# Kernel tuning notes

Measured on AMD Instinct MI355X. Metric: run time of the kernel, lower is better.

Reference implementation:

```python
import jax, jax.numpy as jnp
import numpy as np

B, T, S, O = 8, 60, 36, 1
H, E, PE = 4, 16, 16
AD, TA, OUT, L = 12, 10, 64, 2
PRUNE_KEEP_FROM = int(np.floor(S * S * 0.5))  # floor(S^2 * (1 - prune_rate))
EPS = 1e-5


def lrelu(v):
    return jax.nn.leaky_relu(v, 0.01)


def pos_encode(times):
    # standard sinusoidal PE on raw timestamps -> (B, T, PE)
    half = PE // 2
    div = jnp.exp(jnp.arange(half, dtype=jnp.float32) * (-jnp.log(10000.0) / half))
    ang = times[..., None] * div
    return jnp.stack([jnp.sin(ang), jnp.cos(ang)], axis=-1).reshape(times.shape + (PE,))


def pair_sim(adj):
    # sum_{i<j} ||a_i - a_j||^2 = B*sum_i||a_i||^2 - ||sum_i a_i||^2
    b = adj.shape[0]
    sq = jnp.sum(adj * adj)
    tot = jnp.sum(adj, axis=0)
    return (b * sq - jnp.sum(tot * tot)) / ((b - 1) ** 2) / (S * S)


def _forward(x, times, mask, bn_g, bn_b, obs_emb_w, attn_w, bidir_w, proj_W, proj_b,
             Wq, bq, Wk, bk, Ws, bs, lnt_g, lnt_b, Wse, bse, lns_g, lns_b):
    b = x.shape[0]
    # BatchNorm2d over timestep channels (training-mode batch stats)
    mu = x.mean(axis=(0, 2, 3), keepdims=True)
    var = x.var(axis=(0, 2, 3), keepdims=True)
    x = (x - mu) / jnp.sqrt(var + EPS) * bn_g[None, :, None, None] + bn_b[None, :, None, None]
    # per-sensor observation embedding: (B,T,S,O) x (S,O,E*H) -> (B,H,T,S,E)
    h = lrelu(jnp.einsum('btso,som->btsm', x, obs_emb_w))
    h = h.reshape(b, T, S, H, E).transpose(0, 3, 1, 2, 4)
    h = h * mask[:, None, :, :, None]
    pe = pos_encode(times)  # (B,T,PE)
    adj = jnp.ones((b, H, S, S), x.dtype)
    sim = pair_sim(adj)  # 0 for all-ones init, kept for faithfulness
    prune_msk = None
    for lay in range(L):
        hp = h @ proj_W.T + proj_b  # (B,H,T,S,AD+PE)
        cat = jnp.concatenate([
            jnp.broadcast_to(attn_w[lay][None, :, None], (b, H, T, S, AD)),
            jnp.broadcast_to(pe[:, None, :, None], (b, H, T, S, PE))], axis=-1)
        alpha = lrelu(jnp.einsum('bhtsd,bhtjd->bhtsj', hp, cat))  # (B,H,T,S,S)
        if lay:
            cnt = mask.sum(axis=1)[:, None, :, None]  # (B,1,S,1)
            adj = lrelu(adj * (alpha.sum(axis=2) / cnt))
            if prune_msk is None:
                flat = adj.reshape(b, H, S * S)
                ranks = jnp.argsort(jnp.argsort(flat, axis=-1), axis=-1)
                prune_msk = (ranks >= PRUNE_KEEP_FROM).astype(adj.dtype).reshape(b, H, S, S)
            adj = adj * prune_msk
            sim = sim + pair_sim(adj)
        bidir = lrelu(jnp.einsum('hsd,hjd->hsj', bidir_w[lay], bidir_w[lay]))  # (H,S,S)
        w = lrelu(bidir[None, :, None] * alpha * adj[:, :, None])  # (B,H,T,S,S)
        # broadcast message passing: (B,H,T,1,S,E) * (B,H,T,S,S,1) -> sum over source sensor
        h = lrelu(jnp.sum(lrelu(h[:, :, :, None, :, :] * w[..., None]), axis=4))
    pe_e = jnp.broadcast_to(pe[:, None, :, None], (b, H, T, S, PE))
    Hc = jnp.concatenate([h, pe_e], axis=-1).transpose(0, 1, 3, 2, 4)  # (B,H,S,T,E+PE)
    Q = Hc @ Wq.T + bq
    K = Hc @ Wk.T + bk
    beta = jnp.einsum('bhstd,bhsud->bhstu', Q, K)  # (B,H,S,T,T)
    beta = (beta @ Ws.T + bs)[..., 0]  # (B,H,S,T)
    m = beta.mean(axis=(-2, -1), keepdims=True)
    v = beta.var(axis=(-2, -1), keepdims=True)
    beta = (beta - m) / jnp.sqrt(v + EPS) * lnt_g + lnt_b
    out = lrelu(jnp.einsum('bhst,bhstd->bhsd', beta, Hc))
    out = lrelu(out @ Wse.T + bse)
    m2 = out.mean(axis=(-2, -1), keepdims=True)
    v2 = out.var(axis=(-2, -1), keepdims=True)
    out = (out - m2) / jnp.sqrt(v2 + EPS) * lns_g + lns_b
    out = out.transpose(0, 2, 1, 3).reshape(b, S, OUT)
    return out, sim


def setup_inputs():
    key = jax.random.key(0)
    ks = jax.random.split(key, 12)
    def rn(k, shape, scale=0.1):
        return jax.random.normal(k, shape, jnp.float32) * scale
    return {
        'x': jax.random.normal(ks[0], (B, T, S, O), jnp.float32),
        'times': jnp.tile(jnp.arange(T, dtype=jnp.float32), (B, 1)),
        'mask': jnp.ones((B, T, S), jnp.float32),
        'bn_g': jnp.ones((T,), jnp.float32),
        'bn_b': jnp.zeros((T,), jnp.float32),
        'obs_emb_w': rn(ks[1], (S, O, E * H)),
        'attn_w': rn(ks[2], (L, H, S, AD)),
        'bidir_w': rn(ks[3], (L, H, S, AD)),
        'proj_W': rn(ks[4], (AD + PE, E)),
        'proj_b': jnp.zeros((AD + PE,), jnp.float32),
        'Wq': rn(ks[5], (TA, E + PE)),
        'bq': jnp.zeros((TA,), jnp.float32),
        'Wk': rn(ks[6], (TA, E + PE)),
        'bk': jnp.zeros((TA,), jnp.float32),
        'Ws': rn(ks[7], (1, T)),
        'bs': jnp.zeros((1,), jnp.float32),
        'lnt_g': jnp.ones((S, T), jnp.float32),
        'lnt_b': jnp.zeros((S, T), jnp.float32),
        'Wse': rn(ks[8], (OUT // H, E + PE)),
        'bse': jnp.zeros((OUT // H,), jnp.float32),
        'lns_g': jnp.ones((S, OUT // H), jnp.float32),
        'lns_b': jnp.zeros((S, OUT // H), jnp.float32),
    }


def reference(x, times, mask, bn_g, bn_b, obs_emb_w, attn_w, bidir_w, proj_W, proj_b,
              Wq, bq, Wk, bk, Ws, bs, lnt_g, lnt_b, Wse, bse, lns_g, lns_b):
    return _forward(x, times, mask, bn_g, bn_b, obs_emb_w, attn_w, bidir_w, proj_W, proj_b,
                    Wq, bq, Wk, bk, Ws, bs, lnt_g, lnt_b, Wse, bse, lns_g, lns_b)
```

## Files before the change

### kernel.cpp

```cpp
#include <hip/hip_runtime.h>
#include <math.h>

#define Bc 8
#define Tc 60
#define Sc 36
#define Hc_ 4
#define Ec 16
#define PEc 16
#define ADc 12
#define TAc 10
#define OUTc 64
#define KEEP 648
#define EPSc 1e-5f
#define LOG1E4_8 1.15129254649702284f

#define WS_H2     18176
#define WS_H1     1124096
#define WS_ALPHA  2230016
#define WS_ADJ    4759808
#define WS_ADJP   4801280
#define WS_CNT    5050112
#define WS_BETA   WS_ALPHA
#define WS_PART   (WS_ALPHA + 69120)
#define WS_OUT2   (WS_ALPHA + 71424)
#define WS_PART2  (WS_ALPHA + 89856)

__device__ __forceinline__ float lrelu(float v){ return v >= 0.f ? v : 0.01f*v; }

__global__ __launch_bounds__(256) void k_layer01(const float* __restrict__ x,
                          const float* __restrict__ times,
                          const float* __restrict__ mask,
                          const float* __restrict__ bn_g,
                          const float* __restrict__ bn_b,
                          const float* __restrict__ obs_w,
                          const float* __restrict__ attn,
                          const float* __restrict__ bidw,
                          const float* __restrict__ projW,
                          const float* __restrict__ projb,
                          float* __restrict__ ws){
    int idx = blockIdx.x;
    int t = idx % Tc; int bh = idx / Tc; int h = bh % Hc_; int b = bh / Hc_;
    int tid = threadIdx.x;
    __shared__ float sh_h[Sc*Ec];
    __shared__ float sh_h1[Sc*Ec];
    __shared__ float sh_pe[PEc];
    __shared__ float sh_at0T[ADc*Sc];
    __shared__ float sh_at1T[ADc*Sc];
    __shared__ float sh_bwT[ADc*Sc];
    __shared__ float sh_hp[Sc*28];
    __shared__ float sh_P[Sc];
    __shared__ float sh_w[Sc*Sc];
    __shared__ float sh_xn[Sc];
    __shared__ float sh_m[Sc];
    __shared__ float sred[8];
    float s0 = 0.f, s1 = 0.f;
    for (int i = tid; i < Bc*Sc; i += 256){
        float v = x[((i/Sc)*Tc + t)*Sc + (i%Sc)];
        s0 += v; s1 += v*v;
    }
    #pragma unroll
    for (int off = 32; off; off >>= 1){
        s0 += __shfl_down(s0, off, 64);
        s1 += __shfl_down(s1, off, 64);
    }
    if ((tid & 63) == 0){ sred[(tid>>6)*2] = s0; sred[(tid>>6)*2 + 1] = s1; }
    if (tid >= 64 && tid < 80){
        int q = tid - 64; int j = q >> 1;
        float ang = times[b*Tc + t] * expf(-(float)j * LOG1E4_8);
        sh_pe[q] = (q & 1) ? cosf(ang) : sinf(ang);
    }
    for (int i = tid; i < ADc*Sc; i += 256){
        int d = i / Sc, j = i % Sc;
        sh_at0T[i] = attn[h*Sc*ADc + j*ADc + d];
        sh_at1T[i] = attn[(Hc_ + h)*Sc*ADc + j*ADc + d];
        sh_bwT[i]  = bidw[h*Sc*ADc + j*ADc + d];
    }
    __syncthreads();
    float mu  = (sred[0]+sred[2]+sred[4]+sred[6]) / (float)(Bc*Sc);
    float var = (sred[1]+sred[3]+sred[5]+sred[7]) / (float)(Bc*Sc) - mu*mu;
    if (tid < Sc){
        float xv = x[(b*Tc + t)*Sc + tid];
        sh_xn[tid] = (xv - mu) * rsqrtf(var + EPSc) * bn_g[t] + bn_b[t];
        sh_m[tid]  = mask[(b*Tc + t)*Sc + tid];
    }
    __syncthreads();
    for (int i = tid; i < Sc*Ec; i += 256){
        int s = i / Ec, e = i % Ec;
        sh_h[i] = lrelu(sh_xn[s]*obs_w[s*64 + h*Ec + e]) * sh_m[s];
    }
    __syncthreads();
    for (int i = tid; i < Sc*28; i += 256){
        int s = i / 28, d = i % 28;
        float acc = projb[d];
        const float* w = projW + d*Ec;
        const float* hh = sh_h + s*Ec;
        #pragma unroll
        for (int e = 0; e < Ec; e++) acc += hh[e]*w[e];
        sh_hp[i] = acc;
    }
    __syncthreads();
    if (tid < Sc){
        const float* hp = sh_hp + tid*28 + ADc;
        float p = 0.f;
        #pragma unroll
        for (int d = 0; d < PEc; d++) p += hp[d]*sh_pe[d];
        sh_P[tid] = p;
    }
    __syncthreads();
    for (int i = tid; i < Sc*Sc; i += 256){
        int s = i / Sc, j = i % Sc;
        const float* hp = sh_hp + s*28;
        float acc = sh_P[s];
        float bd = 0.f;
        #pragma unroll
        for (int d = 0; d < ADc; d++){
            acc += hp[d]*sh_at0T[d*Sc + j];
            bd  += sh_bwT[d*Sc + s]*sh_bwT[d*Sc + j];
        }
        sh_w[i] = lrelu(lrelu(bd)*lrelu(acc));
    }
    __syncthreads();
    float* h1g = ws + WS_H1 + (size_t)idx*Sc*Ec;
    for (int i = tid; i < Sc*Ec; i += 256){
        int s = i / Ec, e = i % Ec;
        float acc = 0.f;
        #pragma unroll 6
        for (int j = 0; j < Sc; j++) acc += lrelu(sh_h[j*Ec + e]*sh_w[s*Sc + j]);
        float v = lrelu(acc);
        sh_h1[i] = v;
        h1g[i] = v;
    }
    __syncthreads();
    for (int i = tid; i < Sc*28; i += 256){
        int s = i / 28, d = i % 28;
        float acc = projb[d];
        const float* w = projW + d*Ec;
        const float* hh = sh_h1 + s*Ec;
        #pragma unroll
        for (int e = 0; e < Ec; e++) acc += hh[e]*w[e];
        sh_hp[i] = acc;
    }
    __syncthreads();
    if (tid < Sc){
        const float* hp = sh_hp + tid*28 + ADc;
        float p = 0.f;
        #pragma unroll
        for (int d = 0; d < PEc; d++) p += hp[d]*sh_pe[d];
        sh_P[tid] = p;
    }
    __syncthreads();
    float* adst = ws + WS_ALPHA + (size_t)idx*Sc*Sc;
    for (int i = tid; i < Sc*Sc; i += 256){
        int s = i / Sc, j = i % Sc;
        const float* hp = sh_hp + s*28;
        float acc = sh_P[s];
        #pragma unroll
        for (int d = 0; d < ADc; d++) acc += hp[d]*sh_at1T[d*Sc + j];
        adst[i] = lrelu(acc);
    }
}

__global__ __launch_bounds__(256) void k_adjpart(const float* __restrict__ mask, float* __restrict__ ws){
    int bh = blockIdx.x / 6; int chunk = blockIdx.x % 6;
    int tid = threadIdx.x;
    const float4* a = (const float4*)(ws + WS_ALPHA + (size_t)bh*Tc*Sc*Sc) + (size_t)chunk*10*324;
    float4* p = (float4*)(ws + WS_ADJP + (size_t)blockIdx.x*Sc*Sc);
    for (int c = tid; c < 324; c += 256){
        float4 acc = make_float4(0.f, 0.f, 0.f, 0.f);
        #pragma unroll
        for (int tt = 0; tt < 10; tt++){
            float4 u = a[(size_t)tt*324 + c];
            acc.x += u.x; acc.y += u.y; acc.z += u.z; acc.w += u.w;
        }
        p[c] = acc;
    }
    if (chunk == 0 && (bh & 3) == 0 && tid < Sc){
        int b = bh >> 2;
        float c = 0.f;
        #pragma unroll 4
        for (int t = 0; t < Tc; t++) c += mask[(b*Tc + t)*Sc + tid];
        ws[WS_CNT + b*Sc + tid] = c;
    }
}

__global__ __launch_bounds__(256) void k_prune(float* __restrict__ ws){
    int bh = blockIdx.x / 24; int chunk = blockIdx.x % 24;
    int b = bh >> 2;
    int tid = threadIdx.x;
    __shared__ __align__(16) float sh_v[Sc*Sc];
    __shared__ float sh_cnt[Sc];
    const float4* p = (const float4*)(ws + WS_ADJP + (size_t)bh*6*Sc*Sc);
    for (int c = tid; c < 324; c += 256){
        float4 acc = make_float4(0.f, 0.f, 0.f, 0.f);
        #pragma unroll
        for (int q = 0; q < 6; q++){
            float4 u = p[(size_t)q*324 + c];
            acc.x += u.x; acc.y += u.y; acc.z += u.z; acc.w += u.w;
        }
        ((float4*)sh_v)[c] = acc;
    }
    if (tid < Sc) sh_cnt[tid] = ws[WS_CNT + b*Sc + tid];
    __syncthreads();
    for (int i = tid; i < Sc*Sc; i += 256){
        int s = i / Sc;
        sh_v[i] = lrelu(sh_v[i] / sh_cnt[s]);
    }
    __syncthreads();
    int r = tid >> 2; if (r > 53) r = 53;
    int part = tid & 3;
    int i = chunk*54 + r;
    float v = sh_v[i];
    const float4* v4 = (const float4*)sh_v + part*81;
    int a0 = part*324;
    int cnt = 0;
    #pragma unroll 9
    for (int j = 0; j < 81; j++){
        float4 u = v4[j];
        int k = a0 + j*4;
        cnt += (int)(u.x < v) + ((int)(u.x == v) & (int)(k   < i));
        cnt += (int)(u.y < v) + ((int)(u.y == v) & (int)(k+1 < i));
        cnt += (int)(u.z < v) + ((int)(u.z == v) & (int)(k+2 < i));
        cnt += (int)(u.w < v) + ((int)(u.w == v) & (int)(k+3 < i));
    }
    cnt += __shfl_down(cnt, 2, 4);
    cnt += __shfl_down(cnt, 1, 4);
    if (part == 0 && tid < 216)
        ws[WS_ADJ + bh*Sc*Sc + i] = (cnt >= KEEP) ? v : 0.f;
}

__global__ __launch_bounds__(256) void k_layer1mp(const float* __restrict__ bidw,
                                                  float* __restrict__ ws){
    int idx = blockIdx.x;
    int bh = idx / Tc; int h = bh % Hc_;
    int tid = threadIdx.x;
    __shared__ float sh_h[Sc*Ec];
    __shared__ float sh_w[Sc*Sc];
    __shared__ float sh_bwT[ADc*Sc];
    const float* hsrc = ws + WS_H1 + (size_t)idx*Sc*Ec;
    float*       hdst = ws + WS_H2 + (size_t)idx*Sc*Ec;
    const float* al  = ws + WS_ALPHA + (size_t)idx*Sc*Sc;
    const float* adj = ws + WS_ADJ + bh*Sc*Sc;
    for (int i = tid; i < Sc*Ec; i += 256) sh_h[i] = hsrc[i];
    for (int i = tid; i < ADc*Sc; i += 256){
        int d = i / Sc, j = i % Sc;
        sh_bwT[i] = bidw[(Hc_ + h)*Sc*ADc + j*ADc + d];
    }
    __syncthreads();
    for (int i = tid; i < Sc*Sc; i += 256){
        int s = i / Sc, j = i % Sc;
        float bd = 0.f;
        #pragma unroll
        for (int d = 0; d < ADc; d++) bd += sh_bwT[d*Sc + s]*sh_bwT[d*Sc + j];
        sh_w[i] = lrelu(lrelu(bd)*al[i]*adj[i]);
    }
    __syncthreads();
    for (int i = tid; i < Sc*Ec; i += 256){
        int s = i / Ec, e = i % Ec;
        float acc = 0.f;
        #pragma unroll 6
        for (int j = 0; j < Sc; j++) acc += lrelu(sh_h[j*Ec + e]*sh_w[s*Sc + j]);
        hdst[i] = lrelu(acc);
    }
}

__global__ __launch_bounds__(64) void kF1(const float* __restrict__ Wq, const float* __restrict__ bq,
                   const float* __restrict__ Wk, const float* __restrict__ bk,
                   const float* __restrict__ Ws_, const float* __restrict__ bs_,
                   const float* __restrict__ times, float* __restrict__ ws){
    int idx = blockIdx.x;
    int s = idx % Sc; int bh = idx / Sc; int b = bh / Hc_;
    int tid = threadIdx.x;
    __shared__ float sh_Hc[Tc*33];
    __shared__ float sh_K[Tc*11];
    __shared__ float sh_Wq[TAc*32];
    __shared__ float sh_WkT[32*TAc];
    __shared__ float sh_bq[TAc], sh_bk[TAc];
    __shared__ float sh_ws[Tc];
    __shared__ float sh_Kw[TAc];
    const float* h2 = ws + WS_H2 + (size_t)bh*Tc*Sc*Ec + s*Ec;
    for (int i4 = tid; i4 < Tc*4; i4 += 64){
        int t = i4 >> 2, c4 = i4 & 3;
        float4 u = *(const float4*)(h2 + t*Sc*Ec + c4*4);
        float* d = sh_Hc + t*33 + c4*4;
        d[0] = u.x; d[1] = u.y; d[2] = u.z; d[3] = u.w;
    }
    for (int i = tid; i < Tc*PEc; i += 64){
        int t = i / PEc, q = i % PEc; int j = q >> 1;
        float ang = times[b*Tc + t] * expf(-(float)j * LOG1E4_8);
        sh_Hc[t*33 + Ec + q] = (q & 1) ? cosf(ang) : sinf(ang);
    }
    for (int i = tid; i < TAc*32; i += 64){
        sh_Wq[i] = Wq[i];
        int d = i / 32, q = i % 32;
        sh_WkT[q*TAc + d] = Wk[i];
    }
    if (tid < TAc){ sh_bq[tid] = bq[tid]; sh_bk[tid] = bk[tid]; }
    if (tid < Tc) sh_ws[tid] = Ws_[tid];
    __syncthreads();
    for (int i = tid; i < Tc*TAc; i += 64){
        int t = i / TAc, d = i % TAc;
        const float* hc = sh_Hc + t*33;
        float acc = sh_bk[d];
        #pragma unroll
        for (int q = 0; q < 32; q++) acc += hc[q]*sh_WkT[q*TAc + d];
        sh_K[t*11 + d] = acc;
    }
    __syncthreads();
    if (tid < TAc){
        float acc = 0.f;
        #pragma unroll 4
        for (int t = 0; t < Tc; t++) acc += sh_K[t*11 + tid]*sh_ws[t];
        sh_Kw[tid] = acc;
    }
    __syncthreads();
    float bv = 0.f;
    float bsv = bs_[0];
    if (tid < Tc){
        const float* hc = sh_Hc + tid*33;
        float acc = bsv;
        #pragma unroll
        for (int d = 0; d < TAc; d++){
            const float* wq = sh_Wq + d*32;
            float qv = sh_bq[d];
            #pragma unroll
            for (int q = 0; q < 32; q++) qv += hc[q]*wq[q];
            acc += qv*sh_Kw[d];
        }
        bv = acc;
        ws[WS_BETA + idx*Tc + tid] = acc;
    }
    float p0 = (tid < Tc) ? bv : 0.f;
    float p1 = p0*bv;
    #pragma unroll
    for (int off = 32; off; off >>= 1){
        p0 += __shfl_down(p0, off, 64);
        p1 += __shfl_down(p1, off, 64);
    }
    if (tid == 0){
        ws[WS_PART + idx*2]     = p0;
        ws[WS_PART + idx*2 + 1] = p1;
    }
}

__global__ __launch_bounds__(64) void kF2(const float* __restrict__ lnt_g, const float* __restrict__ lnt_b,
                   const float* __restrict__ Wse, const float* __restrict__ bse,
                   const float* __restrict__ times, float* __restrict__ ws){
    int idx = blockIdx.x;
    int s = idx % Sc; int bh = idx / Sc; int b = bh / Hc_;
    int tid = threadIdx.x;
    __shared__ float sh_Hc[Tc*33];
    __shared__ float sh_beta[Tc];
    __shared__ float sh_o1[32];
    __shared__ float sh_mi[2];
    float p0 = 0.f, p1 = 0.f;
    if (tid < Sc){
        p0 = ws[WS_PART + (bh*Sc + tid)*2];
        p1 = ws[WS_PART + (bh*Sc + tid)*2 + 1];
    }
    #pragma unroll
    for (int off = 32; off; off >>= 1){
        p0 += __shfl_down(p0, off, 64);
        p1 += __shfl_down(p1, off, 64);
    }
    if (tid == 0){
        float m = p0 / (float)(Sc*Tc);
        sh_mi[0] = m;
        sh_mi[1] = rsqrtf(p1 / (float)(Sc*Tc) - m*m + EPSc);
    }
    const float* h2 = ws + WS_H2 + (size_t)bh*Tc*Sc*Ec + s*Ec;
    for (int i4 = tid; i4 < Tc*4; i4 += 64){
        int t = i4 >> 2, c4 = i4 & 3;
        float4 u = *(const float4*)(h2 + t*Sc*Ec + c4*4);
        float* d = sh_Hc + t*33 + c4*4;
        d[0] = u.x; d[1] = u.y; d[2] = u.z; d[3] = u.w;
    }
    for (int i = tid; i < Tc*PEc; i += 64){
        int t = i / PEc, q = i % PEc; int j = q >> 1;
        float ang = times[b*Tc + t] * expf(-(float)j * LOG1E4_8);
        sh_Hc[t*33 + Ec + q] = (q & 1) ? cosf(ang) : sinf(ang);
    }
    __syncthreads();
    float m = sh_mi[0], inv = sh_mi[1];
    if (tid < Tc){
        float bvv = ws[WS_BETA + idx*Tc + tid];
        sh_beta[tid] = (bvv - m)*inv*lnt_g[s*Tc + tid] + lnt_b[s*Tc + tid];
    }
    __syncthreads();
    if (tid < 32){
        float acc = 0.f;
        #pragma unroll 4
        for (int t = 0; t < Tc; t++) acc += sh_beta[t]*sh_Hc[t*33 + tid];
        sh_o1[tid] = lrelu(acc);
    }
    __syncthreads();
    float v = 0.f;
    if (tid < 16){
        float acc = bse[tid];
        const float* w = Wse + tid*32;
        #pragma unroll
        for (int d = 0; d < 32; d++) acc += sh_o1[d]*w[d];
        v = lrelu(acc);
        ws[WS_OUT2 + idx*16 + tid] = v;
    }
    float q0 = v, q1 = v*v;
    #pragma unroll
    for (int off = 32; off; off >>= 1){
        q0 += __shfl_down(q0, off, 64);
        q1 += __shfl_down(q1, off, 64);
    }
    if (tid == 0){
        ws[WS_PART2 + idx*2]     = q0;
        ws[WS_PART2 + idx*2 + 1] = q1;
    }
}

__global__ __launch_bounds__(256) void kF3s(const float* __restrict__ lns_g, const float* __restrict__ lns_b,
                    const float* __restrict__ ws, float* __restrict__ out){
    int tid = threadIdx.x;
    if (blockIdx.x == 32){
        float sq = 0.f, t2 = 0.f;
        for (int i = tid; i < Hc_*Sc*Sc; i += 256){
            float tot = 0.f;
            #pragma unroll
            for (int b = 0; b < Bc; b++){
                float v = ws[WS_ADJ + b*Hc_*Sc*Sc + i];
                sq += v*v; tot += v;
            }
            t2 += tot*tot;
        }
        __shared__ float r0[256], r1[256];
        r0[tid] = sq; r1[tid] = t2; __syncthreads();
        for (int off = 128; off; off >>= 1){
            if (tid < off){ r0[tid] += r0[tid+off]; r1[tid] += r1[tid+off]; }
            __syncthreads();
        }
        if (tid == 0)
            out[Bc*Sc*OUTc] = ((float)Bc*r0[0] - r1[0]) / 49.f / 1296.f;
        return;
    }
    int bh = blockIdx.x; int h = bh % Hc_; int b = bh / Hc_;
    __shared__ float sh_mi[2];
    if (tid < 64){
        float p0 = 0.f, p1 = 0.f;
        if (tid < Sc){
            p0 = ws[WS_PART2 + (bh*Sc + tid)*2];
            p1 = ws[WS_PART2 + (bh*Sc + tid)*2 + 1];
        }
        #pragma unroll
        for (int off = 32; off; off >>= 1){
            p0 += __shfl_down(p0, off, 64);
            p1 += __shfl_down(p1, off, 64);
        }
        if (tid == 0){
            float m = p0 / (float)(Sc*16);
            sh_mi[0] = m;
            sh_mi[1] = rsqrtf(p1 / (float)(Sc*16) - m*m + EPSc);
        }
    }
    __syncthreads();
    float m2 = sh_mi[0], inv2 = sh_mi[1];
    for (int i = tid; i < Sc*16; i += 256){
        int s = i / 16, k = i % 16;
        float v = ws[WS_OUT2 + bh*Sc*16 + i];
        out[(b*Sc + s)*OUTc + h*16 + k] = (v - m2)*inv2*lns_g[i] + lns_b[i];
    }
}

extern "C" void kernel_launch(void* const* d_in, const int* in_sizes, int n_in,
                              void* d_out, int out_size, void* d_ws, size_t ws_size,
                              hipStream_t stream){
    const float* x     = (const float*)d_in[0];
    const float* times = (const float*)d_in[1];
    const float* mask  = (const float*)d_in[2];
    const float* bn_g  = (const float*)d_in[3];
    const float* bn_b  = (const float*)d_in[4];
    const float* obs   = (const float*)d_in[5];
    const float* attn  = (const float*)d_in[6];
    const float* bidw  = (const float*)d_in[7];
    const float* projW = (const float*)d_in[8];
    const float* projb = (const float*)d_in[9];
    const float* Wq    = (const float*)d_in[10];
    const float* bq    = (const float*)d_in[11];
    const float* Wk    = (const float*)d_in[12];
    const float* bk    = (const float*)d_in[13];
    const float* Ws_   = (const float*)d_in[14];
    const float* bs_   = (const float*)d_in[15];
    const float* lnt_g = (const float*)d_in[16];
    const float* lnt_b = (const float*)d_in[17];
    const float* Wse   = (const float*)d_in[18];
    const float* bse   = (const float*)d_in[19];
    const float* lns_g = (const float*)d_in[20];
    const float* lns_b = (const float*)d_in[21];
    float* ws  = (float*)d_ws;
    float* out = (float*)d_out;

    k_layer01<<<Bc*Hc_*Tc, 256, 0, stream>>>(x, times, mask, bn_g, bn_b, obs, attn, bidw, projW, projb, ws);
    k_adjpart<<<Bc*Hc_*6, 256, 0, stream>>>(mask, ws);
    k_prune<<<Bc*Hc_*24, 256, 0, stream>>>(ws);
    k_layer1mp<<<Bc*Hc_*Tc, 256, 0, stream>>>(bidw, ws);
    kF1<<<Bc*Hc_*Sc, 64, 0, stream>>>(Wq, bq, Wk, bk, Ws_, bs_, times, ws);
    kF2<<<Bc*Hc_*Sc, 64, 0, stream>>>(lnt_g, lnt_b, Wse, bse, times, ws);
    kF3s<<<Bc*Hc_ + 1, 256, 0, stream>>>(lns_g, lns_b, ws, out);
}
```

Measured before the change: 207.3 us.

## Fuse seven stage kernels into one persistent cooperative kernel with grid syncs

Replaces the chain of seven kernel launches with a single cooperative kernel of 512 persistent blocks that loops over each stage's work items and separates stages with grid-wide syncs. The goal is to remove per-launch overhead and inter-kernel gaps, which matter because each stage is small. In exchange, each stage runs on a fixed 512-block grid with a grid barrier between stages, and occupancy is capped by launch bounds and a large static shared-memory buffer. If the cooperative launch fails, it falls back to the original multi-kernel path.

```diff
diff --git a/kernel.cpp b/kernel.cpp
--- a/kernel.cpp
+++ b/kernel.cpp
@@ -1,5 +1,8 @@
 #include <hip/hip_runtime.h>
+#include <hip/hip_cooperative_groups.h>
 #include <math.h>
+
+namespace cg = cooperative_groups;
 
 #define Bc 8
 #define Tc 60
@@ -25,7 +28,456 @@
 #define WS_OUT2   (WS_ALPHA + 71424)
 #define WS_PART2  (WS_ALPHA + 89856)
 
+#define GRIDN 512
+
+#define P5_WQ   0
+#define P5_WKT  320
+#define P5_BQ   640
+#define P5_BK   650
+#define P5_WS   660
+#define P5_WAVE 720
+#define SMEM_FLOATS 11392
+
 __device__ __forceinline__ float lrelu(float v){ return v >= 0.f ? v : 0.01f*v; }
+
+__global__ __launch_bounds__(256, 2) void k_fused(
+    const float* __restrict__ x, const float* __restrict__ times,
+    const float* __restrict__ mask, const float* __restrict__ bn_g,
+    const float* __restrict__ bn_b, const float* __restrict__ obs_w,
+    const float* __restrict__ attn, const float* __restrict__ bidw,
+    const float* __restrict__ projW, const float* __restrict__ projb,
+    const float* __restrict__ Wq, const float* __restrict__ bq,
+    const float* __restrict__ Wk, const float* __restrict__ bk,
+    const float* __restrict__ Ws_, const float* __restrict__ bs_,
+    const float* __restrict__ lnt_g, const float* __restrict__ lnt_b,
+    const float* __restrict__ Wse, const float* __restrict__ bse,
+    const float* __restrict__ lns_g, const float* __restrict__ lns_b,
+    float* __restrict__ ws, float* __restrict__ out)
+{
+    cg::grid_group gridg = cg::this_grid();
+    int tid = threadIdx.x;
+    int wid = tid >> 6, lane = tid & 63;
+    __shared__ __align__(16) float smem[SMEM_FLOATS];
+
+    {
+        float* sh_h    = smem;
+        float* sh_h1   = smem + 576;
+        float* sh_pe   = smem + 1152;
+        float* sh_at0T = smem + 1168;
+        float* sh_at1T = smem + 1600;
+        float* sh_bwT  = smem + 2032;
+        float* sh_hp   = smem + 2464;
+        float* sh_P    = smem + 3472;
+        float* sh_w    = smem + 3508;
+        float* sh_xn   = smem + 4804;
+        float* sh_m    = smem + 4840;
+        float* sred    = smem + 4876;
+        for (int u = blockIdx.x; u < Bc*Hc_*Tc; u += GRIDN){
+            __syncthreads();
+            int t = u % Tc; int bh0 = u / Tc; int h = bh0 % Hc_; int b = bh0 / Hc_;
+            float s0 = 0.f, s1 = 0.f;
+            for (int i = tid; i < Bc*Sc; i += 256){
+                float v = x[((i/Sc)*Tc + t)*Sc + (i%Sc)];
+                s0 += v; s1 += v*v;
+            }
+            #pragma unroll
+            for (int off = 32; off; off >>= 1){
+                s0 += __shfl_down(s0, off, 64);
+                s1 += __shfl_down(s1, off, 64);
+            }
+            if ((tid & 63) == 0){ sred[(tid>>6)*2] = s0; sred[(tid>>6)*2 + 1] = s1; }
+            if (tid >= 64 && tid < 80){
+                int q = tid - 64; int j = q >> 1;
+                float ang = times[b*Tc + t] * expf(-(float)j * LOG1E4_8);
+                sh_pe[q] = (q & 1) ? cosf(ang) : sinf(ang);
+            }
+            for (int i = tid; i < ADc*Sc; i += 256){
+                int d = i / Sc, j = i % Sc;
+                sh_at0T[i] = attn[h*Sc*ADc + j*ADc + d];
+                sh_at1T[i] = attn[(Hc_ + h)*Sc*ADc + j*ADc + d];
+                sh_bwT[i]  = bidw[h*Sc*ADc + j*ADc + d];
+            }
+            __syncthreads();
+            float mu  = (sred[0]+sred[2]+sred[4]+sred[6]) / (float)(Bc*Sc);
+            float var = (sred[1]+sred[3]+sred[5]+sred[7]) / (float)(Bc*Sc) - mu*mu;
+            if (tid < Sc){
+                float xv = x[(b*Tc + t)*Sc + tid];
+                sh_xn[tid] = (xv - mu) * rsqrtf(var + EPSc) * bn_g[t] + bn_b[t];
+                sh_m[tid]  = mask[(b*Tc + t)*Sc + tid];
+            }
+            __syncthreads();
+            for (int i = tid; i < Sc*Ec; i += 256){
+                int s = i / Ec, e = i % Ec;
+                sh_h[i] = lrelu(sh_xn[s]*obs_w[s*64 + h*Ec + e]) * sh_m[s];
+            }
+            __syncthreads();
+            for (int i = tid; i < Sc*28; i += 256){
+                int s = i / 28, d = i % 28;
+                float acc = projb[d];
+                const float* w = projW + d*Ec;
+                const float* hh = sh_h + s*Ec;
+                #pragma unroll
+                for (int e = 0; e < Ec; e++) acc += hh[e]*w[e];
+                sh_hp[i] = acc;
+            }
+            __syncthreads();
+            if (tid < Sc){
+                const float* hp = sh_hp + tid*28 + ADc;
+                float p = 0.f;
+                #pragma unroll
+                for (int d = 0; d < PEc; d++) p += hp[d]*sh_pe[d];
+                sh_P[tid] = p;
+            }
+            __syncthreads();
+            for (int i = tid; i < Sc*Sc; i += 256){
+                int s = i / Sc, j = i % Sc;
+                const float* hp = sh_hp + s*28;
+                float acc = sh_P[s];
+                float bd = 0.f;
+                #pragma unroll
+                for (int d = 0; d < ADc; d++){
+                    acc += hp[d]*sh_at0T[d*Sc + j];
+                    bd  += sh_bwT[d*Sc + s]*sh_bwT[d*Sc + j];
+                }
+                sh_w[i] = lrelu(lrelu(bd)*lrelu(acc));
+            }
+            __syncthreads();
+            float* h1g = ws + WS_H1 + (size_t)u*Sc*Ec;
+            for (int i = tid; i < Sc*Ec; i += 256){
+                int s = i / Ec, e = i % Ec;
+                float acc = 0.f;
+                #pragma unroll 6
+                for (int j = 0; j < Sc; j++) acc += lrelu(sh_h[j*Ec + e]*sh_w[s*Sc + j]);
+                float v = lrelu(acc);
+                sh_h1[i] = v;
+                h1g[i] = v;
+            }
+            __syncthreads();
+            for (int i = tid; i < Sc*28; i += 256){
+                int s = i / 28, d = i % 28;
+                float acc = projb[d];
+                const float* w = projW + d*Ec;
+                const float* hh = sh_h1 + s*Ec;
+                #pragma unroll
+                for (int e = 0; e < Ec; e++) acc += hh[e]*w[e];
+                sh_hp[i] = acc;
+            }
+            __syncthreads();
+            if (tid < Sc){
+                const float* hp = sh_hp + tid*28 + ADc;
+                float p = 0.f;
+                #pragma unroll
+                for (int d = 0; d < PEc; d++) p += hp[d]*sh_pe[d];
+                sh_P[tid] = p;
+            }
+            __syncthreads();
+            float* adst = ws + WS_ALPHA + (size_t)u*Sc*Sc;
+            for (int i = tid; i < Sc*Sc; i += 256){
+                int s = i / Sc, j = i % Sc;
+                const float* hp = sh_hp + s*28;
+                float acc = sh_P[s];
+                #pragma unroll
+                for (int d = 0; d < ADc; d++) acc += hp[d]*sh_at1T[d*Sc + j];
+                adst[i] = lrelu(acc);
+            }
+        }
+    }
+    gridg.sync();
+
+    for (int u = blockIdx.x; u < Bc*Hc_*6; u += GRIDN){
+        int bh0 = u / 6; int chunk = u % 6;
+        const float4* a = (const float4*)(ws + WS_ALPHA + (size_t)bh0*Tc*Sc*Sc) + (size_t)chunk*10*324;
+        float4* p = (float4*)(ws + WS_ADJP + (size_t)u*Sc*Sc);
+        for (int c = tid; c < 324; c += 256){
+            float4 acc = make_float4(0.f, 0.f, 0.f, 0.f);
+            #pragma unroll
+            for (int tt = 0; tt < 10; tt++){
+                float4 uu = a[(size_t)tt*324 + c];
+                acc.x += uu.x; acc.y += uu.y; acc.z += uu.z; acc.w += uu.w;
+            }
+            p[c] = acc;
+        }
+        if (chunk == 0 && (bh0 & 3) == 0 && tid < Sc){
+            int b = bh0 >> 2;
+            float c = 0.f;
+            #pragma unroll 4
+            for (int t = 0; t < Tc; t++) c += mask[(b*Tc + t)*Sc + tid];
+            ws[WS_CNT + b*Sc + tid] = c;
+        }
+    }
+    gridg.sync();
+
+    {
+        float* sh_v   = smem;
+        float* sh_cnt = smem + 1296;
+        for (int u = blockIdx.x; u < Bc*Hc_*24; u += GRIDN){
+            __syncthreads();
+            int bh0 = u / 24; int chunk = u % 24;
+            int b = bh0 >> 2;
+            const float4* p = (const float4*)(ws + WS_ADJP + (size_t)bh0*6*Sc*Sc);
+            for (int c = tid; c < 324; c += 256){
+                float4 acc = make_float4(0.f, 0.f, 0.f, 0.f);
+                #pragma unroll
+                for (int q = 0; q < 6; q++){
+                    float4 uu = p[(size_t)q*324 + c];
+                    acc.x += uu.x; acc.y += uu.y; acc.z += uu.z; acc.w += uu.w;
+                }
+                ((float4*)sh_v)[c] = acc;
+            }
+            if (tid < Sc) sh_cnt[tid] = ws[WS_CNT + b*Sc + tid];
+            __syncthreads();
+            for (int i = tid; i < Sc*Sc; i += 256){
+                int s = i / Sc;
+                sh_v[i] = lrelu(sh_v[i] / sh_cnt[s]);
+            }
+            __syncthreads();
+            int r = tid >> 2; if (r > 53) r = 53;
+            int part = tid & 3;
+            int i = chunk*54 + r;
+            float v = sh_v[i];
+            const float4* v4 = (const float4*)sh_v + part*81;
+            int a0 = part*324;
+            int cnt = 0;
+            #pragma unroll 9
+            for (int j = 0; j < 81; j++){
+                float4 uu = v4[j];
+                int k = a0 + j*4;
+                cnt += (int)(uu.x < v) + ((int)(uu.x == v) & (int)(k   < i));
+                cnt += (int)(uu.y < v) + ((int)(uu.y == v) & (int)(k+1 < i));
+                cnt += (int)(uu.z < v) + ((int)(uu.z == v) & (int)(k+2 < i));
+                cnt += (int)(uu.w < v) + ((int)(uu.w == v) & (int)(k+3 < i));
+            }
+            cnt += __shfl_down(cnt, 2, 4);
+            cnt += __shfl_down(cnt, 1, 4);
+            if (part == 0 && tid < 216)
+                ws[WS_ADJ + bh0*Sc*Sc + i] = (cnt >= KEEP) ? v : 0.f;
+        }
+    }
+    gridg.sync();
+
+    {
+        float* sh_h   = smem;
+        float* sh_w   = smem + 576;
+        float* sh_bwT = smem + 1872;
+        for (int u = blockIdx.x; u < Bc*Hc_*Tc; u += GRIDN){
+            __syncthreads();
+            int bh0 = u / Tc; int h = bh0 % Hc_;
+            const float* hsrc = ws + WS_H1 + (size_t)u*Sc*Ec;
+            float*       hdst = ws + WS_H2 + (size_t)u*Sc*Ec;
+            const float* al   = ws + WS_ALPHA + (size_t)u*Sc*Sc;
+            const float* adj  = ws + WS_ADJ + bh0*Sc*Sc;
+            for (int i = tid; i < Sc*Ec; i += 256) sh_h[i] = hsrc[i];
+            for (int i = tid; i < ADc*Sc; i += 256){
+                int d = i / Sc, j = i % Sc;
+                sh_bwT[i] = bidw[(Hc_ + h)*Sc*ADc + j*ADc + d];
+            }
+            __syncthreads();
+            for (int i = tid; i < Sc*Sc; i += 256){
+                int s = i / Sc, j = i % Sc;
+                float bd = 0.f;
+                #pragma unroll
+                for (int d = 0; d < ADc; d++) bd += sh_bwT[d*Sc + s]*sh_bwT[d*Sc + j];
+                sh_w[i] = lrelu(lrelu(bd)*al[i]*adj[i]);
+            }
+            __syncthreads();
+            for (int i = tid; i < Sc*Ec; i += 256){
+                int s = i / Ec, e = i % Ec;
+                float acc = 0.f;
+                #pragma unroll 6
+                for (int j = 0; j < Sc; j++) acc += lrelu(sh_h[j*Ec + e]*sh_w[s*Sc + j]);
+                hdst[i] = lrelu(acc);
+            }
+        }
+    }
+    gridg.sync();
+
+    {
+        __syncthreads();
+        for (int i = tid; i < TAc*32; i += 256){
+            smem[P5_WQ + i] = Wq[i];
+            int d = i / 32, q = i % 32;
+            smem[P5_WKT + q*TAc + d] = Wk[i];
+        }
+        if (tid < TAc){ smem[P5_BQ + tid] = bq[tid]; smem[P5_BK + tid] = bk[tid]; }
+        for (int i = tid; i < Tc; i += 256) smem[P5_WS + i] = Ws_[i];
+        __syncthreads();
+        float* W_Hc = smem + P5_WAVE + wid*2656;
+        float* W_K  = W_Hc + 1980;
+        float* W_Kw = W_Hc + 2640;
+        for (int u = blockIdx.x; u < 288; u += GRIDN){
+            int idx = u*4 + wid;
+            int s = idx % Sc; int bh0 = idx / Sc; int b = bh0 / Hc_;
+            const float* h2 = ws + WS_H2 + (size_t)bh0*Tc*Sc*Ec + s*Ec;
+            for (int i4 = lane; i4 < Tc*4; i4 += 64){
+                int t = i4 >> 2, c4 = i4 & 3;
+                float4 uu = *(const float4*)(h2 + t*Sc*Ec + c4*4);
+                float* d = W_Hc + t*33 + c4*4;
+                d[0] = uu.x; d[1] = uu.y; d[2] = uu.z; d[3] = uu.w;
+            }
+            for (int i = lane; i < Tc*PEc; i += 64){
+                int t = i / PEc, q = i % PEc; int j = q >> 1;
+                float ang = times[b*Tc + t] * expf(-(float)j * LOG1E4_8);
+                W_Hc[t*33 + Ec + q] = (q & 1) ? cosf(ang) : sinf(ang);
+            }
+            __syncthreads();
+            for (int i = lane; i < Tc*TAc; i += 64){
+                int t = i / TAc, d = i % TAc;
+                const float* hc = W_Hc + t*33;
+                float acc = smem[P5_BK + d];
+                #pragma unroll
+                for (int q = 0; q < 32; q++) acc += hc[q]*smem[P5_WKT + q*TAc + d];
+                W_K[t*11 + d] = acc;
+            }
+            __syncthreads();
+            if (lane < TAc){
+                float acc = 0.f;
+                #pragma unroll 4
+                for (int t = 0; t < Tc; t++) acc += W_K[t*11 + lane]*smem[P5_WS + t];
+                W_Kw[lane] = acc;
+            }
+            __syncthreads();
+            float bv = 0.f;
+            float bsv = bs_[0];
+            if (lane < Tc){
+                const float* hc = W_Hc + lane*33;
+                float acc = bsv;
+                #pragma unroll
+                for (int d = 0; d < TAc; d++){
+                    const float* wq = smem + P5_WQ + d*32;
+                    float qv = smem[P5_BQ + d];
+                    #pragma unroll
+                    for (int q = 0; q < 32; q++) qv += hc[q]*wq[q];
+                    acc += qv*W_Kw[d];
+                }
+                bv = acc;
+                ws[WS_BETA + idx*Tc + lane] = acc;
+            }
+            float p0 = (lane < Tc) ? bv : 0.f;
+            float p1 = p0*bv;
+            #pragma unroll
+            for (int off = 32; off; off >>= 1){
+                p0 += __shfl_down(p0, off, 64);
+                p1 += __shfl_down(p1, off, 64);
+            }
+            if (lane == 0){
+                ws[WS_PART + idx*2]     = p0;
+                ws[WS_PART + idx*2 + 1] = p1;
+            }
+        }
+    }
+    gridg.sync();
+
+    {
+        float* W_Hc   = smem + P5_WAVE + wid*2656;
+        float* W_beta = W_Hc + 1980;
+        float* W_o1   = W_Hc + 2040;
+        float* W_mi   = W_Hc + 2072;
+        for (int u = blockIdx.x; u < 288; u += GRIDN){
+            int idx = u*4 + wid;
+            int s = idx % Sc; int bh0 = idx / Sc;
+            float p0 = 0.f, p1 = 0.f;
+            if (lane < Sc){
+                p0 = ws[WS_PART + (bh0*Sc + lane)*2];
+                p1 = ws[WS_PART + (bh0*Sc + lane)*2 + 1];
+            }
+            #pragma unroll
+            for (int off = 32; off; off >>= 1){
+                p0 += __shfl_down(p0, off, 64);
+                p1 += __shfl_down(p1, off, 64);
+            }
+            if (lane == 0){
+                float m = p0 / (float)(Sc*Tc);
+                W_mi[0] = m;
+                W_mi[1] = rsqrtf(p1 / (float)(Sc*Tc) - m*m + EPSc);
+            }
+            __syncthreads();
+            float m = W_mi[0], inv = W_mi[1];
+            if (lane < Tc){
+                float bvv = ws[WS_BETA + idx*Tc + lane];
+                W_beta[lane] = (bvv - m)*inv*lnt_g[s*Tc + lane] + lnt_b[s*Tc + lane];
+            }
+            __syncthreads();
+            if (lane < 32){
+                float acc = 0.f;
+                #pragma unroll 4
+                for (int t = 0; t < Tc; t++) acc += W_beta[t]*W_Hc[t*33 + lane];
+                W_o1[lane] = lrelu(acc);
+            }
+            __syncthreads();
+            float v = 0.f;
+            if (lane < 16){
+                float acc = bse[lane];
+                const float* w = Wse + lane*32;
+                #pragma unroll
+                for (int d = 0; d < 32; d++) acc += W_o1[d]*w[d];
+                v = lrelu(acc);
+                ws[WS_OUT2 + idx*16 + lane] = v;
+            }
+            float q0 = v, q1 = v*v;
+            #pragma unroll
+            for (int off = 32; off; off >>= 1){
+                q0 += __shfl_down(q0, off, 64);
+                q1 += __shfl_down(q1, off, 64);
+            }
+            if (lane == 0){
+                ws[WS_PART2 + idx*2]     = q0;
+                ws[WS_PART2 + idx*2 + 1] = q1;
+            }
+        }
+    }
+    gridg.sync();
+
+    for (int u = blockIdx.x; u < Bc*Hc_ + 1; u += GRIDN){
+        __syncthreads();
+        if (u == 32){
+            float sq = 0.f, t2 = 0.f;
+            for (int i = tid; i < Hc_*Sc*Sc; i += 256){
+                float tot = 0.f;
+                #pragma unroll
+                for (int b = 0; b < Bc; b++){
+                    float v = ws[WS_ADJ + b*Hc_*Sc*Sc + i];
+                    sq += v*v; tot += v;
+                }
+                t2 += tot*tot;
+            }
+            float* r0 = smem; float* r1 = smem + 256;
+            r0[tid] = sq; r1[tid] = t2; __syncthreads();
+            for (int off = 128; off; off >>= 1){
+                if (tid < off){ r0[tid] += r0[tid+off]; r1[tid] += r1[tid+off]; }
+                __syncthreads();
+            }
+            if (tid == 0)
+                out[Bc*Sc*OUTc] = ((float)Bc*r0[0] - r1[0]) / 49.f / 1296.f;
+        } else {
+            int bh0 = u; int h = bh0 % Hc_; int b = bh0 / Hc_;
+            float* sh_mi = smem + 512;
+            if (tid < 64){
+                float p0 = 0.f, p1 = 0.f;
+                if (tid < Sc){
+                    p0 = ws[WS_PART2 + (bh0*Sc + tid)*2];
+                    p1 = ws[WS_PART2 + (bh0*Sc + tid)*2 + 1];
+                }
+                #pragma unroll
+                for (int off = 32; off; off >>= 1){
+                    p0 += __shfl_down(p0, off, 64);
+                    p1 += __shfl_down(p1, off, 64);
+                }
+                if (tid == 0){
+                    float m = p0 / (float)(Sc*16);
+                    sh_mi[0] = m;
+                    sh_mi[1] = rsqrtf(p1 / (float)(Sc*16) - m*m + EPSc);
+                }
+            }
+            __syncthreads();
+            float m2 = sh_mi[0], inv2 = sh_mi[1];
+            for (int i = tid; i < Sc*16; i += 256){
+                int s = i / 16, k = i % 16;
+                float v = ws[WS_OUT2 + bh0*Sc*16 + i];
+                out[(b*Sc + s)*OUTc + h*16 + k] = (v - m2)*inv2*lns_g[i] + lns_b[i];
+            }
+        }
+    }
+}
 
 __global__ __launch_bounds__(256) void k_layer01(const float* __restrict__ x,
                           const float* __restrict__ times,
@@ -494,11 +946,20 @@
     float* ws  = (float*)d_ws;
     float* out = (float*)d_out;
 
-    k_layer01<<<Bc*Hc_*Tc, 256, 0, stream>>>(x, times, mask, bn_g, bn_b, obs, attn, bidw, projW, projb, ws);
-    k_adjpart<<<Bc*Hc_*6, 256, 0, stream>>>(mask, ws);
-    k_prune<<<Bc*Hc_*24, 256, 0, stream>>>(ws);
-    k_layer1mp<<<Bc*Hc_*Tc, 256, 0, stream>>>(bidw, ws);
-    kF1<<<Bc*Hc_*Sc, 64, 0, stream>>>(Wq, bq, Wk, bk, Ws_, bs_, times, ws);
-    kF2<<<Bc*Hc_*Sc, 64, 0, stream>>>(lnt_g, lnt_b, Wse, bse, times, ws);
-    kF3s<<<Bc*Hc_ + 1, 256, 0, stream>>>(lns_g, lns_b, ws, out);
+    void* args[] = { (void*)&x, (void*)&times, (void*)&mask, (void*)&bn_g, (void*)&bn_b,
+                     (void*)&obs, (void*)&attn, (void*)&bidw, (void*)&projW, (void*)&projb,
+                     (void*)&Wq, (void*)&bq, (void*)&Wk, (void*)&bk, (void*)&Ws_, (void*)&bs_,
+                     (void*)&lnt_g, (void*)&lnt_b, (void*)&Wse, (void*)&bse, (void*)&lns_g, (void*)&lns_b,
+                     (void*)&ws, (void*)&out };
+    hipError_t err = hipLaunchCooperativeKernel(reinterpret_cast<void*>(k_fused),
+                                                dim3(GRIDN), dim3(256), args, 0, stream);
+    if (err != hipSuccess){
+        k_layer01<<<Bc*Hc_*Tc, 256, 0, stream>>>(x, times, mask, bn_g, bn_b, obs, attn, bidw, projW, projb, ws);
+        k_adjpart<<<Bc*Hc_*6, 256, 0, stream>>>(mask, ws);
+        k_prune<<<Bc*Hc_*24, 256, 0, stream>>>(ws);
+        k_layer1mp<<<Bc*Hc_*Tc, 256, 0, stream>>>(bidw, ws);
+        kF1<<<Bc*Hc_*Sc, 64, 0, stream>>>(Wq, bq, Wk, bk, Ws_, bs_, times, ws);
+        kF2<<<Bc*Hc_*Sc, 64, 0, stream>>>(lnt_g, lnt_b, Wse, bse, times, ws);
+        kF3s<<<Bc*Hc_ + 1, 256, 0, stream>>>(lns_g, lns_b, ws, out);
+    }
 }
```

After: 527.3 us. 154% more time.

## Fuse layer-1 message passing into kF1 and cache positional encodings in workspace

Applied to the files above, without the earlier changes.

Removes the separate k_layer1mp launch. Its message passing now runs inside the per-(b,h,s) kF1 block, which computes the h2 row for its sensor across all timesteps and writes it into shared memory for the Q/K stage. k_layer01 now stores the positional encodings in the workspace so kF1m and kF2 load them instead of recomputing sin/cos. In exchange, each 64-thread block reads its alpha and h1 data with strided global loads (h1 is read straight from global memory inside the inner loop), so access coalescing may be poorer than in the old per-timestep kernel.

```diff
diff --git a/kernel.cpp b/kernel.cpp
--- a/kernel.cpp
+++ b/kernel.cpp
@@ -20,6 +20,7 @@
 #define WS_ADJ    4759808
 #define WS_ADJP   4801280
 #define WS_CNT    5050112
+#define WS_PE     5050496
 #define WS_BETA   WS_ALPHA
 #define WS_PART   (WS_ALPHA + 69120)
 #define WS_OUT2   (WS_ALPHA + 71424)
@@ -67,7 +68,9 @@
     if (tid >= 64 && tid < 80){
         int q = tid - 64; int j = q >> 1;
         float ang = times[b*Tc + t] * expf(-(float)j * LOG1E4_8);
-        sh_pe[q] = (q & 1) ? cosf(ang) : sinf(ang);
+        float pv = (q & 1) ? cosf(ang) : sinf(ang);
+        sh_pe[q] = pv;
+        if (h == 0) ws[WS_PE + (b*Tc + t)*PEc + q] = pv;
     }
     for (int i = tid; i < ADc*Sc; i += 256){
         int d = i / Sc, j = i % Sc;
@@ -228,66 +231,38 @@
         ws[WS_ADJ + bh*Sc*Sc + i] = (cnt >= KEEP) ? v : 0.f;
 }
 
-__global__ __launch_bounds__(256) void k_layer1mp(const float* __restrict__ bidw,
-                                                  float* __restrict__ ws){
-    int idx = blockIdx.x;
-    int bh = idx / Tc; int h = bh % Hc_;
-    int tid = threadIdx.x;
-    __shared__ float sh_h[Sc*Ec];
-    __shared__ float sh_w[Sc*Sc];
-    __shared__ float sh_bwT[ADc*Sc];
-    const float* hsrc = ws + WS_H1 + (size_t)idx*Sc*Ec;
-    float*       hdst = ws + WS_H2 + (size_t)idx*Sc*Ec;
-    const float* al  = ws + WS_ALPHA + (size_t)idx*Sc*Sc;
-    const float* adj = ws + WS_ADJ + bh*Sc*Sc;
-    for (int i = tid; i < Sc*Ec; i += 256) sh_h[i] = hsrc[i];
-    for (int i = tid; i < ADc*Sc; i += 256){
-        int d = i / Sc, j = i % Sc;
-        sh_bwT[i] = bidw[(Hc_ + h)*Sc*ADc + j*ADc + d];
-    }
-    __syncthreads();
-    for (int i = tid; i < Sc*Sc; i += 256){
-        int s = i / Sc, j = i % Sc;
-        float bd = 0.f;
-        #pragma unroll
-        for (int d = 0; d < ADc; d++) bd += sh_bwT[d*Sc + s]*sh_bwT[d*Sc + j];
-        sh_w[i] = lrelu(lrelu(bd)*al[i]*adj[i]);
-    }
-    __syncthreads();
-    for (int i = tid; i < Sc*Ec; i += 256){
-        int s = i / Ec, e = i % Ec;
-        float acc = 0.f;
-        #pragma unroll 6
-        for (int j = 0; j < Sc; j++) acc += lrelu(sh_h[j*Ec + e]*sh_w[s*Sc + j]);
-        hdst[i] = lrelu(acc);
-    }
-}
-
-__global__ __launch_bounds__(64) void kF1(const float* __restrict__ Wq, const float* __restrict__ bq,
+__global__ __launch_bounds__(64) void kF1m(const float* __restrict__ bidw,
+                   const float* __restrict__ Wq, const float* __restrict__ bq,
                    const float* __restrict__ Wk, const float* __restrict__ bk,
                    const float* __restrict__ Ws_, const float* __restrict__ bs_,
-                   const float* __restrict__ times, float* __restrict__ ws){
+                   float* __restrict__ ws){
     int idx = blockIdx.x;
-    int s = idx % Sc; int bh = idx / Sc; int b = bh / Hc_;
+    int s = idx % Sc; int bh = idx / Sc; int h = bh % Hc_; int b = bh / Hc_;
     int tid = threadIdx.x;
     __shared__ float sh_Hc[Tc*33];
+    __shared__ float sh_w[Tc*Sc];
+    __shared__ float sh_bd[Sc];
+    __shared__ float sh_adj[Sc];
     __shared__ float sh_K[Tc*11];
     __shared__ float sh_Wq[TAc*32];
     __shared__ float sh_WkT[32*TAc];
     __shared__ float sh_bq[TAc], sh_bk[TAc];
     __shared__ float sh_ws[Tc];
     __shared__ float sh_Kw[TAc];
-    const float* h2 = ws + WS_H2 + (size_t)bh*Tc*Sc*Ec + s*Ec;
+
     for (int i4 = tid; i4 < Tc*4; i4 += 64){
         int t = i4 >> 2, c4 = i4 & 3;
-        float4 u = *(const float4*)(h2 + t*Sc*Ec + c4*4);
-        float* d = sh_Hc + t*33 + c4*4;
+        float4 u = *(const float4*)(ws + WS_PE + (size_t)(b*Tc + t)*PEc + c4*4);
+        float* d = sh_Hc + t*33 + Ec + c4*4;
         d[0] = u.x; d[1] = u.y; d[2] = u.z; d[3] = u.w;
     }
-    for (int i = tid; i < Tc*PEc; i += 64){
-        int t = i / PEc, q = i % PEc; int j = q >> 1;
-        float ang = times[b*Tc + t] * expf(-(float)j * LOG1E4_8);
-        sh_Hc[t*33 + Ec + q] = (q & 1) ? cosf(ang) : sinf(ang);
+    if (tid < Sc){
+        const float* bw = bidw + (Hc_ + h)*Sc*ADc;
+        float bd = 0.f;
+        #pragma unroll
+        for (int d = 0; d < ADc; d++) bd += bw[s*ADc + d]*bw[tid*ADc + d];
+        sh_bd[tid]  = lrelu(bd);
+        sh_adj[tid] = ws[WS_ADJ + bh*Sc*Sc + s*Sc + tid];
     }
     for (int i = tid; i < TAc*32; i += 64){
         sh_Wq[i] = Wq[i];
@@ -296,6 +271,26 @@
     }
     if (tid < TAc){ sh_bq[tid] = bq[tid]; sh_bk[tid] = bk[tid]; }
     if (tid < Tc) sh_ws[tid] = Ws_[tid];
+    __syncthreads();
+    const float* al = ws + WS_ALPHA + (size_t)bh*Tc*Sc*Sc + s*Sc;
+    for (int i = tid; i < Tc*Sc; i += 64){
+        int t = i / Sc, j = i % Sc;
+        sh_w[i] = lrelu(sh_bd[j]*al[(size_t)t*Sc*Sc + j]*sh_adj[j]);
+    }
+    __syncthreads();
+    const float* h1 = ws + WS_H1 + (size_t)bh*Tc*Sc*Ec;
+    float*       h2 = ws + WS_H2 + (size_t)bh*Tc*Sc*Ec;
+    for (int i = tid; i < Tc*Ec; i += 64){
+        int t = i / Ec, e = i % Ec;
+        const float* hr = h1 + (size_t)t*Sc*Ec + e;
+        const float* wr = sh_w + t*Sc;
+        float acc = 0.f;
+        #pragma unroll 6
+        for (int j = 0; j < Sc; j++) acc += lrelu(hr[j*Ec]*wr[j]);
+        float v = lrelu(acc);
+        sh_Hc[t*33 + e] = v;
+        h2[(size_t)(t*Sc + s)*Ec + e] = v;
+    }
     __syncthreads();
     for (int i = tid; i < Tc*TAc; i += 64){
         int t = i / TAc, d = i % TAc;
@@ -344,7 +339,7 @@
 
 __global__ __launch_bounds__(64) void kF2(const float* __restrict__ lnt_g, const float* __restrict__ lnt_b,
                    const float* __restrict__ Wse, const float* __restrict__ bse,
-                   const float* __restrict__ times, float* __restrict__ ws){
+                   float* __restrict__ ws){
     int idx = blockIdx.x;
     int s = idx % Sc; int bh = idx / Sc; int b = bh / Hc_;
     int tid = threadIdx.x;
@@ -374,10 +369,11 @@
         float* d = sh_Hc + t*33 + c4*4;
         d[0] = u.x; d[1] = u.y; d[2] = u.z; d[3] = u.w;
     }
-    for (int i = tid; i < Tc*PEc; i += 64){
-        int t = i / PEc, q = i % PEc; int j = q >> 1;
-        float ang = times[b*Tc + t] * expf(-(float)j * LOG1E4_8);
-        sh_Hc[t*33 + Ec + q] = (q & 1) ? cosf(ang) : sinf(ang);
+    for (int i4 = tid; i4 < Tc*4; i4 += 64){
+        int t = i4 >> 2, c4 = i4 & 3;
+        float4 u = *(const float4*)(ws + WS_PE + (size_t)(b*Tc + t)*PEc + c4*4);
+        float* d = sh_Hc + t*33 + Ec + c4*4;
+        d[0] = u.x; d[1] = u.y; d[2] = u.z; d[3] = u.w;
     }
     __syncthreads();
     float m = sh_mi[0], inv = sh_mi[1];
@@ -497,8 +493,7 @@
     k_layer01<<<Bc*Hc_*Tc, 256, 0, stream>>>(x, times, mask, bn_g, bn_b, obs, attn, bidw, projW, projb, ws);
     k_adjpart<<<Bc*Hc_*6, 256, 0, stream>>>(mask, ws);
     k_prune<<<Bc*Hc_*24, 256, 0, stream>>>(ws);
-    k_layer1mp<<<Bc*Hc_*Tc, 256, 0, stream>>>(bidw, ws);
-    kF1<<<Bc*Hc_*Sc, 64, 0, stream>>>(Wq, bq, Wk, bk, Ws_, bs_, times, ws);
-    kF2<<<Bc*Hc_*Sc, 64, 0, stream>>>(lnt_g, lnt_b, Wse, bse, times, ws);
+    kF1m<<<Bc*Hc_*Sc, 64, 0, stream>>>(bidw, Wq, bq, Wk, bk, Ws_, bs_, ws);
+    kF2<<<Bc*Hc_*Sc, 64, 0, stream>>>(lnt_g, lnt_b, Wse, bse, ws);
     kF3s<<<Bc*Hc_ + 1, 256, 0, stream>>>(lns_g, lns_b, ws, out);
 }
```

Result: slower. 233.7 us (+12.7%).

## Transpose H2 workspace to sensor-major layout and cache positional encoding

Applied to the files above, without the earlier changes.

k_layer1mp now writes its output in (b,h,s,t,e) order, so kF1 and kF2 read a contiguous block of T*E floats per sensor instead of strided rows. k_layer01 stores the sinusoidal positional encoding to workspace once, and kF1/kF2 load it with float4 reads instead of recomputing expf/sinf/cosf per block. lrelu becomes a branchless fmaxf. The writes from k_layer1mp become strided across t, which trades write coalescing for read coalescing downstream.

```diff
diff --git a/kernel.cpp b/kernel.cpp
--- a/kernel.cpp
+++ b/kernel.cpp
@@ -20,12 +20,13 @@
 #define WS_ADJ    4759808
 #define WS_ADJP   4801280
 #define WS_CNT    5050112
+#define WS_PE     5050496
 #define WS_BETA   WS_ALPHA
 #define WS_PART   (WS_ALPHA + 69120)
 #define WS_OUT2   (WS_ALPHA + 71424)
 #define WS_PART2  (WS_ALPHA + 89856)
 
-__device__ __forceinline__ float lrelu(float v){ return v >= 0.f ? v : 0.01f*v; }
+__device__ __forceinline__ float lrelu(float v){ return fmaxf(v, 0.01f*v); }
 
 __global__ __launch_bounds__(256) void k_layer01(const float* __restrict__ x,
                           const float* __restrict__ times,
@@ -67,7 +68,9 @@
     if (tid >= 64 && tid < 80){
         int q = tid - 64; int j = q >> 1;
         float ang = times[b*Tc + t] * expf(-(float)j * LOG1E4_8);
-        sh_pe[q] = (q & 1) ? cosf(ang) : sinf(ang);
+        float pv = (q & 1) ? cosf(ang) : sinf(ang);
+        sh_pe[q] = pv;
+        if (h == 0) ws[WS_PE + (b*Tc + t)*PEc + q] = pv;
     }
     for (int i = tid; i < ADc*Sc; i += 256){
         int d = i / Sc, j = i % Sc;
@@ -231,13 +234,12 @@
 __global__ __launch_bounds__(256) void k_layer1mp(const float* __restrict__ bidw,
                                                   float* __restrict__ ws){
     int idx = blockIdx.x;
-    int bh = idx / Tc; int h = bh % Hc_;
+    int t = idx % Tc; int bh = idx / Tc; int h = bh % Hc_;
     int tid = threadIdx.x;
     __shared__ float sh_h[Sc*Ec];
     __shared__ float sh_w[Sc*Sc];
     __shared__ float sh_bwT[ADc*Sc];
     const float* hsrc = ws + WS_H1 + (size_t)idx*Sc*Ec;
-    float*       hdst = ws + WS_H2 + (size_t)idx*Sc*Ec;
     const float* al  = ws + WS_ALPHA + (size_t)idx*Sc*Sc;
     const float* adj = ws + WS_ADJ + bh*Sc*Sc;
     for (int i = tid; i < Sc*Ec; i += 256) sh_h[i] = hsrc[i];
@@ -259,16 +261,16 @@
         float acc = 0.f;
         #pragma unroll 6
         for (int j = 0; j < Sc; j++) acc += lrelu(sh_h[j*Ec + e]*sh_w[s*Sc + j]);
-        hdst[i] = lrelu(acc);
+        ws[WS_H2 + ((size_t)(bh*Sc + s)*Tc + t)*Ec + e] = lrelu(acc);
     }
 }
 
 __global__ __launch_bounds__(64) void kF1(const float* __restrict__ Wq, const float* __restrict__ bq,
                    const float* __restrict__ Wk, const float* __restrict__ bk,
                    const float* __restrict__ Ws_, const float* __restrict__ bs_,
-                   const float* __restrict__ times, float* __restrict__ ws){
+                   float* __restrict__ ws){
     int idx = blockIdx.x;
-    int s = idx % Sc; int bh = idx / Sc; int b = bh / Hc_;
+    int bh = idx / Sc; int b = bh / Hc_;
     int tid = threadIdx.x;
     __shared__ float sh_Hc[Tc*33];
     __shared__ float sh_K[Tc*11];
@@ -277,17 +279,18 @@
     __shared__ float sh_bq[TAc], sh_bk[TAc];
     __shared__ float sh_ws[Tc];
     __shared__ float sh_Kw[TAc];
-    const float* h2 = ws + WS_H2 + (size_t)bh*Tc*Sc*Ec + s*Ec;
+    const float* h2c = ws + WS_H2 + (size_t)idx*Tc*Ec;
     for (int i4 = tid; i4 < Tc*4; i4 += 64){
         int t = i4 >> 2, c4 = i4 & 3;
-        float4 u = *(const float4*)(h2 + t*Sc*Ec + c4*4);
+        float4 u = *(const float4*)(h2c + i4*4);
         float* d = sh_Hc + t*33 + c4*4;
         d[0] = u.x; d[1] = u.y; d[2] = u.z; d[3] = u.w;
     }
-    for (int i = tid; i < Tc*PEc; i += 64){
-        int t = i / PEc, q = i % PEc; int j = q >> 1;
-        float ang = times[b*Tc + t] * expf(-(float)j * LOG1E4_8);
-        sh_Hc[t*33 + Ec + q] = (q & 1) ? cosf(ang) : sinf(ang);
+    for (int i4 = tid; i4 < Tc*4; i4 += 64){
+        int t = i4 >> 2, c4 = i4 & 3;
+        float4 u = *(const float4*)(ws + WS_PE + (size_t)(b*Tc + t)*PEc + c4*4);
+        float* d = sh_Hc + t*33 + Ec + c4*4;
+        d[0] = u.x; d[1] = u.y; d[2] = u.z; d[3] = u.w;
     }
     for (int i = tid; i < TAc*32; i += 64){
         sh_Wq[i] = Wq[i];
@@ -344,7 +347,7 @@
 
 __global__ __launch_bounds__(64) void kF2(const float* __restrict__ lnt_g, const float* __restrict__ lnt_b,
                    const float* __restrict__ Wse, const float* __restrict__ bse,
-                   const float* __restrict__ times, float* __restrict__ ws){
+                   float* __restrict__ ws){
     int idx = blockIdx.x;
     int s = idx % Sc; int bh = idx / Sc; int b = bh / Hc_;
     int tid = threadIdx.x;
@@ -367,17 +370,18 @@
         sh_mi[0] = m;
         sh_mi[1] = rsqrtf(p1 / (float)(Sc*Tc) - m*m + EPSc);
     }
-    const float* h2 = ws + WS_H2 + (size_t)bh*Tc*Sc*Ec + s*Ec;
+    const float* h2c = ws + WS_H2 + (size_t)idx*Tc*Ec;
     for (int i4 = tid; i4 < Tc*4; i4 += 64){
         int t = i4 >> 2, c4 = i4 & 3;
-        float4 u = *(const float4*)(h2 + t*Sc*Ec + c4*4);
+        float4 u = *(const float4*)(h2c + i4*4);
         float* d = sh_Hc + t*33 + c4*4;
         d[0] = u.x; d[1] = u.y; d[2] = u.z; d[3] = u.w;
     }
-    for (int i = tid; i < Tc*PEc; i += 64){
-        int t = i / PEc, q = i % PEc; int j = q >> 1;
-        float ang = times[b*Tc + t] * expf(-(float)j * LOG1E4_8);
-        sh_Hc[t*33 + Ec + q] = (q & 1) ? cosf(ang) : sinf(ang);
+    for (int i4 = tid; i4 < Tc*4; i4 += 64){
+        int t = i4 >> 2, c4 = i4 & 3;
+        float4 u = *(const float4*)(ws + WS_PE + (size_t)(b*Tc + t)*PEc + c4*4);
+        float* d = sh_Hc + t*33 + Ec + c4*4;
+        d[0] = u.x; d[1] = u.y; d[2] = u.z; d[3] = u.w;
     }
     __syncthreads();
     float m = sh_mi[0], inv = sh_mi[1];
@@ -498,7 +502,7 @@
     k_adjpart<<<Bc*Hc_*6, 256, 0, stream>>>(mask, ws);
     k_prune<<<Bc*Hc_*24, 256, 0, stream>>>(ws);
     k_layer1mp<<<Bc*Hc_*Tc, 256, 0, stream>>>(bidw, ws);
-    kF1<<<Bc*Hc_*Sc, 64, 0, stream>>>(Wq, bq, Wk, bk, Ws_, bs_, times, ws);
-    kF2<<<Bc*Hc_*Sc, 64, 0, stream>>>(lnt_g, lnt_b, Wse, bse, times, ws);
+    kF1<<<Bc*Hc_*Sc, 64, 0, stream>>>(Wq, bq, Wk, bk, Ws_, bs_, ws);
+    kF2<<<Bc*Hc_*Sc, 64, 0, stream>>>(lnt_g, lnt_b, Wse, bse, ws);
     kF3s<<<Bc*Hc_ + 1, 256, 0, stream>>>(lns_g, lns_b, ws, out);
 }
```

Result: faster. 201.6 us (-2.8%).
